# Kernel optimization log

Measured on AMD Instinct MI355X. Metric: run time of the kernel, lower is better.

Reference implementation:

```python
import jax, jax.numpy as jnp
import numpy as np

RATE = 2
KSIZE = 3
STRIDE = 1
SOFTMAX_SCALE = 10.0
EPS_NAN = 1e-4


def resize_bilinear_align(x, oh, ow):
    # torch F.interpolate(mode='bilinear', align_corners=True)
    B, C, H, W = x.shape
    ys = jnp.linspace(0.0, H - 1.0, oh)
    xs = jnp.linspace(0.0, W - 1.0, ow)
    y0 = jnp.floor(ys).astype(jnp.int32)
    y1 = jnp.minimum(y0 + 1, H - 1)
    wy = (ys - y0).astype(x.dtype)
    x0 = jnp.floor(xs).astype(jnp.int32)
    x1 = jnp.minimum(x0 + 1, W - 1)
    wx = (xs - x0).astype(x.dtype)
    t = x[:, :, y0, :] * (1 - wy)[None, None, :, None] + x[:, :, y1, :] * wy[None, None, :, None]
    return t[:, :, :, x0] * (1 - wx) + t[:, :, :, x1] * wx


def extract_patches(x, k, s, pad):
    # x: [C,H,W] -> [L, C, k, k] with SAME padding (pad on each side), L = oh*ow
    C, H, W = x.shape
    xp = jnp.pad(x, ((0, 0), (pad, pad), (pad, pad)))
    oh = (H + 2 * pad - k) // s + 1
    ow = (W + 2 * pad - k) // s + 1
    cols = jnp.stack(
        [xp[:, i:i + s * (oh - 1) + 1:s, j:j + s * (ow - 1) + 1:s]
         for i in range(k) for j in range(k)], axis=0)  # [k*k, C, oh, ow]
    return cols.reshape(k, k, C, oh, ow).transpose(3, 4, 2, 0, 1).reshape(oh * ow, C, k, k)


def conv2d(x, w, padding):
    # x: [N,C,H,W], w: [O,I,kh,kw]
    return jax.lax.conv_general_dilated(
        x, w, (1, 1), [(padding, padding)] * 2,
        dimension_numbers=('NCHW', 'OIHW', 'NCHW'))


def conv_transpose2d(x, w, stride, padding):
    # torch conv_transpose2d: x [N,I,h,w], w [I,O,kh,kw]
    k = w.shape[2]
    wt = jnp.flip(w, (2, 3)).transpose(1, 0, 2, 3)  # [O,I,kh,kw]
    return jax.lax.conv_general_dilated(
        x, wt, (1, 1), [(k - 1 - padding, k - 1 - padding)] * 2,
        lhs_dilation=(stride, stride),
        dimension_numbers=('NCHW', 'OIHW', 'NCHW'))


def setup_inputs() -> dict:
    key = jax.random.key(0)
    k1, k2 = jax.random.split(key)
    B, C, H, W = 4, 64, 128, 128
    background = jax.random.normal(k1, (B, C, H, W), dtype=jnp.float32)
    foreground = jax.random.normal(k2, (B, C, H, W), dtype=jnp.float32)
    return {"background": background, "foreground": foreground}


def reference(background, foreground):
    B, C, H, W = background.shape
    h, w = H // RATE, W // RATE
    fg = resize_bilinear_align(foreground, h, w)  # [B,C,h,w]
    bks = 2 * RATE  # background patch kernel = 4

    def per_sample(fg_i, bg_i):
        # foreground patches [L,C,3,3], L = h*w
        fgp = extract_patches(fg_i, KSIZE, STRIDE, 1)
        norm = jnp.sqrt(jnp.sum(fgp * fgp, axis=(1, 2, 3), keepdims=True))
        fgp_n = fgp / jnp.maximum(norm, EPS_NAN)
        # correlation score [1,L,h,w]
        score = conv2d(fg_i[None], fgp_n, padding=1)
        attn = jax.nn.softmax(score * SOFTMAX_SCALE, axis=1)
        attn = jnp.clip(attn, 1e-8, None)
        # background patches [L,C,4,4] (kernel 4, stride 2, same-pad 1)
        bgp = extract_patches(bg_i, bks, STRIDE * RATE, 1)
        out = conv_transpose2d(attn, bgp, stride=RATE, padding=1) / 4.0
        return out[0]  # [C,H,W]

    return jax.vmap(per_sample)(fg, background)
```

## Files before the change

kernel.cpp:

```cpp
#include <hip/hip_runtime.h>
#include <hip/hip_bf16.h>
#include <math.h>

#define B_  4
#define C_  64
#define H_  128
#define W_  128
#define HS  64
#define WS  64
#define L_  4096
#define K1  576
#define E2  1024
#define KSPLIT 1
#define ZLOG (-17.5f)

typedef _Float16 f16;
typedef f16 f16x8 __attribute__((ext_vector_type(8)));
typedef float f32x4 __attribute__((ext_vector_type(4)));

__device__ __forceinline__ void gload16(const void* g, void* l) {
    __builtin_amdgcn_global_load_lds(
        (const __attribute__((address_space(1))) unsigned int*)g,
        (__attribute__((address_space(3))) unsigned int*)l, 16, 0, 0);
}

__device__ __forceinline__ int swz(int r, int c) {
    return r * 128 + ((((c >> 3) ^ (r & 7)) << 3) | (c & 7));
}

__global__ __launch_bounds__(256) void resize_kernel(const float* __restrict__ fg,
                                                     float* __restrict__ fgs) {
    int idx = blockIdx.x * 256 + threadIdx.x;
    if (idx >= B_ * C_ * HS * WS) return;
    int j = idx & 63, i = (idx >> 6) & 63, bc = idx >> 12;
    const float sc = 127.0f / 63.0f;
    float yf = i * sc, xf = j * sc;
    int y0 = (int)floorf(yf); if (y0 > 127) y0 = 127;
    int x0 = (int)floorf(xf); if (x0 > 127) x0 = 127;
    int y1 = min(y0 + 1, 127), x1 = min(x0 + 1, 127);
    float wy = yf - (float)y0, wx = xf - (float)x0;
    const float* p = fg + (size_t)bc * (H_ * W_);
    float a = p[y0 * W_ + x0], b = p[y0 * W_ + x1];
    float c = p[y1 * W_ + x0], d = p[y1 * W_ + x1];
    float t0 = a * (1.f - wy) + c * wy;
    float t1 = b * (1.f - wy) + d * wy;
    fgs[idx] = t0 * (1.f - wx) + t1 * wx;
}

__global__ __launch_bounds__(256) void patch_kernel(const float* __restrict__ fgs,
                                                    f16* __restrict__ P_all) {
    int idx = blockIdx.x * 256 + threadIdx.x;
    int b = blockIdx.y;
    int k = idx % K1, l = idx / K1;
    int c = k / 9, r = k % 9;
    int dy = r / 3, dx = r % 3;
    int ly = l >> 6, lx = l & 63;
    int y = ly - 1 + dy, x = lx - 1 + dx;
    float v = 0.f;
    if ((unsigned)y < 64u && (unsigned)x < 64u)
        v = fgs[((size_t)b * C_ + c) * (HS * WS) + y * WS + x];
    P_all[(size_t)b * L_ * K1 + idx] = (f16)v;
}

__global__ __launch_bounds__(64) void norm_kernel(const f16* __restrict__ P_all,
                                                  float* __restrict__ nrm_all) {
    int l = blockIdx.x, b = blockIdx.y, t = threadIdx.x;
    const f16* row = P_all + ((size_t)b * L_ + l) * K1;
    float s = 0.f;
    for (int k = t; k < K1; k += 64) { float v = (float)row[k]; s = fmaf(v, v, s); }
    #pragma unroll
    for (int off = 32; off; off >>= 1) s += __shfl_down(s, off);
    if (t == 0) nrm_all[b * L_ + l] = fmaxf(sqrtf(s), 1e-4f);
}

__global__ __launch_bounds__(256) void v_kernel(const float* __restrict__ bg_g,
                                                f16* __restrict__ VT_g) {
    int ls = blockIdx.y;
    const float* bg_b = bg_g + (size_t)ls * (C_ * H_ * W_);
    f16* VT = VT_g + (size_t)ls * ((size_t)E2 * L_);
    int idx = blockIdx.x * 256 + threadIdx.x;
    int l = idx & 4095, e = idx >> 12;
    int c = e >> 4, r = e & 15;
    int ky = r >> 2, kx = r & 3;
    int ly = l >> 6, lx = l & 63;
    int by = 2 * ly - 1 + ky, bx = 2 * lx - 1 + kx;
    float v = 0.f;
    if ((unsigned)by < 128u && (unsigned)bx < 128u)
        v = bg_b[(size_t)c * (H_ * W_) + by * W_ + bx];
    VT[idx] = (f16)v;
}

__device__ __forceinline__ int nextk(int kn, int kLen, unsigned long long mask) {
    while (kn < kLen) {
        int t = kn >> 7;
        if (mask & (1ull << t)) return kn;
        unsigned long long m = mask >> t;
        if (!m) return kLen;
        kn = (t + __builtin_ctzll(m)) << 7;
    }
    return kn;
}

template <int EPI>
__global__ __launch_bounds__(512, 4)
void mfma_gemm(const f16* __restrict__ A, size_t sA,
               const f16* __restrict__ Bt, size_t sB,
               int lda, int ldb, int kLen, void* __restrict__ outp, size_t sOut,
               int ldc, const float* __restrict__ nrm, float* __restrict__ rowsum,
               int* __restrict__ flags) {
    __shared__ __align__(16) f16 As[2][2][128 * 32];
    __shared__ __align__(16) f16 Bs[2][2][128 * 32];
    __shared__ float sred[16];

    const int lin = blockIdx.x;
    const int S = gridDim.x >> 3;
    int bx, by, ls;
    if (EPI == 1) {
        int s = (lin & 7) * S + (lin >> 3);
        int R = s / 136, q = s - R * 136;
        ls = R >> 2;
        int rr = R & 3;
        if (rr < 2) {
            int a = 0;
            while (q >= 16 - a) { q -= 16 - a; ++a; }
            by = a + (rr << 4); bx = a + q + (rr << 4);
        } else {
            if (q >= 128) return;
            by = q & 15; bx = 16 + ((rr & 1) << 3) + (q >> 4);
        }
    } else {
        int G = (lin & 7) * S + (lin >> 3);
        ls = G >> 8;
        by = (G >> 5) & 7; bx = G & 31;
    }

    A  += (size_t)ls * sA;
    Bt += (size_t)ls * sB;
    f16* outbase = (f16*)outp + (size_t)ls * sOut;
    if (EPI == 1) { nrm += (size_t)ls * L_; rowsum += (size_t)ls * L_; }
    flags += ls * 1024;

    const int tid = threadIdx.x;
    const int w = tid >> 6, lane = tid & 63;
    const int row0 = by * 128, col0 = bx * 128;

    unsigned long long kmask = ~0ull;
    if (EPI == 0) {
        int f = (lane < 32) ? flags[bx * 32 + lane] : 0;
        kmask = __ballot(f != 0);
    }

    const int srow = tid >> 2;
    const int scol = (((tid & 3) ^ ((tid >> 3) & 3)) * 8);
    const f16* gA = A + (size_t)(row0 + srow) * lda + scol;
    const f16* gB = Bt + (size_t)(col0 + srow) * ldb + scol;
    const int ld = tid * 8;

    const int wm = w >> 2, wn = w & 3;
    const int mfm = lane & 15, quad = lane >> 4;
    const int rq = (quad ^ ((mfm >> 1) & 3)) * 8;
    f32x4 acc[4][2] = {};

    int kc = (EPI == 0) ? nextk(0, kLen, kmask) : 0;
    if (kc < kLen) {
        int cur = 0;
        gload16(gA + kc,      &As[0][0][ld]);
        gload16(gA + kc + 32, &As[0][1][ld]);
        gload16(gB + kc,      &Bs[0][0][ld]);
        gload16(gB + kc + 32, &Bs[0][1][ld]);
        for (;;) {
            int kn = (EPI == 0) ? nextk(kc + 64, kLen, kmask) : kc + 64;
            __builtin_amdgcn_s_barrier();
            if (kn < kLen) {
                const int nxt = cur ^ 1;
                gload16(gA + kn,      &As[nxt][0][ld]);
                gload16(gA + kn + 32, &As[nxt][1][ld]);
                gload16(gB + kn,      &Bs[nxt][0][ld]);
                gload16(gB + kn + 32, &Bs[nxt][1][ld]);
                asm volatile("s_waitcnt vmcnt(4)" ::: "memory");
            } else {
                asm volatile("s_waitcnt vmcnt(0)" ::: "memory");
            }
            __builtin_amdgcn_s_barrier();
            __builtin_amdgcn_sched_barrier(0);
            #pragma unroll
            for (int h = 0; h < 2; ++h) {
                f16x8 af[4], bf[2];
                #pragma unroll
                for (int mi = 0; mi < 4; ++mi)
                    af[mi] = *(const f16x8*)&As[cur][h][(wm * 64 + mi * 16 + mfm) * 32 + rq];
                #pragma unroll
                for (int ni = 0; ni < 2; ++ni)
                    bf[ni] = *(const f16x8*)&Bs[cur][h][(wn * 32 + ni * 16 + mfm) * 32 + rq];
                __builtin_amdgcn_s_setprio(1);
                #pragma unroll
                for (int mi = 0; mi < 4; ++mi)
                    #pragma unroll
                    for (int ni = 0; ni < 2; ++ni)
                        acc[mi][ni] = __builtin_amdgcn_mfma_f32_16x16x32_f16(
                            af[mi], bf[ni], acc[mi][ni], 0, 0, 0);
                __builtin_amdgcn_s_setprio(0);
            }
            cur ^= 1;
            kc = kn;
            if (kc >= kLen) break;
        }
    }

    const int orow = row0 + wm * 64;
    const int ocol = col0 + wn * 32;
    f16* st = &As[0][0][0];

    if (EPI == 1) {
        f16* Eo = outbase;
        const bool offd = (by != bx);
        float rowm[16], csr[16], cs[2], cm2[2];
        #pragma unroll
        for (int j = 0; j < 16; ++j) {
            float n = nrm[orow + (j >> 2) * 16 + quad * 4 + (j & 3)];
            rowm[j] = 10.0f * n; csr[j] = 10.0f / n;
        }
        #pragma unroll
        for (int ni = 0; ni < 2; ++ni) {
            float n = nrm[ocol + ni * 16 + mfm];
            cs[ni] = 10.0f / n; cm2[ni] = 10.0f * n;
        }
        float mx1 = -1e30f, mx2 = -1e30f;
        #pragma unroll
        for (int ni = 0; ni < 2; ++ni)
            #pragma unroll
            for (int mi = 0; mi < 4; ++mi)
                #pragma unroll
                for (int r = 0; r < 4; ++r) {
                    float a = acc[mi][ni][r];
                    mx1 = fmaxf(mx1, a * cs[ni] - rowm[mi * 4 + r]);
                    mx2 = fmaxf(mx2, a * csr[mi * 4 + r] - cm2[ni]);
                }
        #pragma unroll
        for (int off = 32; off; off >>= 1) {
            mx1 = fmaxf(mx1, __shfl_xor(mx1, off));
            mx2 = fmaxf(mx2, __shfl_xor(mx2, off));
        }
        if (lane == 0) { sred[w] = mx1; sred[8 + w] = mx2; }
        __syncthreads();
        float b1 = sred[0], b2 = sred[8];
        #pragma unroll
        for (int k = 1; k < 8; ++k) {
            b1 = fmaxf(b1, sred[k]); b2 = fmaxf(b2, sred[8 + k]);
        }
        int nz1 = b1 > ZLOG;
        int nz2 = offd && (b2 > ZLOG);
        if (nz1) {
            float rs[16] = {};
            #pragma unroll
            for (int ni = 0; ni < 2; ++ni)
                #pragma unroll
                for (int mi = 0; mi < 4; ++mi)
                    #pragma unroll
                    for (int r = 0; r < 4; ++r) {
                        float e = __expf(acc[mi][ni][r] * cs[ni] - rowm[mi * 4 + r]);
                        rs[mi * 4 + r] += e;
                        st[swz(wm * 64 + mi * 16 + quad * 4 + r,
                               wn * 32 + ni * 16 + mfm)] = (f16)e;
                    }
            __syncthreads();
            #pragma unroll
            for (int it = 0; it < 4; ++it) {
                int chunk = it * 512 + tid;
                int row = chunk >> 4, c16 = chunk & 15;
                f16x8 v = *(const f16x8*)&st[row * 128 + ((c16 ^ (row & 7)) << 3)];
                *(f16x8*)&Eo[(size_t)(row0 + row) * ldc + col0 + c16 * 8] = v;
            }
            #pragma unroll
            for (int j = 0; j < 16; ++j) {
                float v = rs[j];
                v += __shfl_xor(v, 1); v += __shfl_xor(v, 2);
                v += __shfl_xor(v, 4); v += __shfl_xor(v, 8);
                if (mfm == 0)
                    atomicAdd(&rowsum[orow + (j >> 2) * 16 + quad * 4 + (j & 3)], v);
            }
        }
        if (nz2) {
            __syncthreads();
            float rs2[2] = {};
            #pragma unroll
            for (int ni = 0; ni < 2; ++ni)
                #pragma unroll
                for (int mi = 0; mi < 4; ++mi)
                    #pragma unroll
                    for (int r = 0; r < 4; ++r) {
                        float e = __expf(acc[mi][ni][r] * csr[mi * 4 + r] - cm2[ni]);
                        rs2[ni] += e;
                        st[swz(wn * 32 + ni * 16 + mfm,
                               wm * 64 + mi * 16 + quad * 4 + r)] = (f16)e;
                    }
            __syncthreads();
            #pragma unroll
            for (int it = 0; it < 4; ++it) {
                int chunk = it * 512 + tid;
                int row = chunk >> 4, c16 = chunk & 15;
                f16x8 v = *(const f16x8*)&st[row * 128 + ((c16 ^ (row & 7)) << 3)];
                *(f16x8*)&Eo[(size_t)(col0 + row) * ldc + row0 + c16 * 8] = v;
            }
            #pragma unroll
            for (int ni = 0; ni < 2; ++ni) {
                float v = rs2[ni];
                v += __shfl_xor(v, 16); v += __shfl_xor(v, 32);
                if (quad == 0)
                    atomicAdd(&rowsum[ocol + ni * 16 + mfm], v);
            }
        }
        if (tid == 0) {
            flags[by * 32 + bx] = nz1;
            if (offd) flags[bx * 32 + by] = nz2;
        }
    } else {
        __syncthreads();
        #pragma unroll
        for (int ni = 0; ni < 2; ++ni)
            #pragma unroll
            for (int mi = 0; mi < 4; ++mi)
                #pragma unroll
                for (int r = 0; r < 4; ++r)
                    st[swz(wm * 64 + mi * 16 + quad * 4 + r,
                           wn * 32 + ni * 16 + mfm)] = (f16)acc[mi][ni][r];
        __syncthreads();
        f16* base = outbase + (size_t)row0 * ldc + col0;
        #pragma unroll
        for (int it = 0; it < 4; ++it) {
            int chunk = it * 512 + tid;
            int row = chunk >> 4, c16 = chunk & 15;
            f16x8 v = *(const f16x8*)&st[row * 128 + ((c16 ^ (row & 7)) << 3)];
            *(f16x8*)&base[(size_t)row * ldc + c16 * 8] = v;
        }
    }
}

__global__ __launch_bounds__(256) void gather_kernel(const f16* __restrict__ OPT_g,
                                                     const float* __restrict__ rowsum_g,
                                                     float* __restrict__ out_g) {
    int ls = blockIdx.y;
    const f16* OPT = OPT_g + (size_t)ls * ((size_t)KSPLIT * E2 * L_);
    const float* rowsum = rowsum_g + (size_t)ls * L_;
    float* out_b = out_g + (size_t)ls * (C_ * H_ * W_);
    int idx = blockIdx.x * 256 + threadIdx.x;
    if (idx >= C_ * H_ * W_) return;
    int X = idx & 127, Y = (idx >> 7) & 127, c = idx >> 14;
    int kyp = (Y + 1) & 1;
    int kxp = (X + 1) & 1;
    float sum = 0.f;
    #pragma unroll
    for (int ky = kyp; ky < 4; ky += 2) {
        int py = (Y + 1 - ky) >> 1;
        if ((unsigned)py >= 64u) continue;
        #pragma unroll
        for (int kx = kxp; kx < 4; kx += 2) {
            int px = (X + 1 - kx) >> 1;
            if ((unsigned)px >= 64u) continue;
            int p = py * 64 + px;
            int e = c * 16 + ky * 4 + kx;
            float v = 0.f;
            #pragma unroll
            for (int s = 0; s < KSPLIT; ++s)
                v += (float)OPT[((size_t)s * E2 + e) * L_ + p];
            sum += v * __builtin_amdgcn_rcpf(rowsum[p]);
        }
    }
    out_b[idx] = 0.25f * sum;
}

extern "C" void kernel_launch(void* const* d_in, const int* in_sizes, int n_in,
                              void* d_out, int out_size, void* d_ws, size_t ws_size,
                              hipStream_t stream) {
    const float* bg = (const float*)d_in[0];
    const float* fg = (const float*)d_in[1];
    float* out = (float*)d_out;
    char* w8 = (char*)d_ws;

    float* fgs        = (float*)(w8);
    f16*   P_all      = (f16*)  (w8 + 4194304);
    float* nrm        = (float*)(w8 + 23068672);
    float* rowsum_all = (float*)(w8 + 23134208);
    int*   flags      = (int*)  (w8 + 23199744);
    const size_t base = 23216128;

    const size_t perVT  = (size_t)E2 * L_ * 2;
    const size_t perEb  = (size_t)L_ * L_ * 2;
    const size_t perOPT = (size_t)KSPLIT * E2 * L_ * 2;
    const size_t per = perVT + perEb + perOPT;
    int nb = 1;
    if (ws_size >= base + 4 * per) nb = 4;
    else if (ws_size >= base + 2 * per) nb = 2;

    f16* VT  = (f16*)(w8 + base);
    f16* Eb  = (f16*)(w8 + base + (size_t)nb * perVT);
    f16* OPT = (f16*)(w8 + base + (size_t)nb * (perVT + perEb));

    resize_kernel<<<(B_ * C_ * HS * WS) / 256, 256, 0, stream>>>(fg, fgs);
    patch_kernel<<<dim3((L_ * K1) / 256, B_), 256, 0, stream>>>(fgs, P_all);
    norm_kernel<<<dim3(L_, B_), 64, 0, stream>>>(P_all, nrm);
    hipMemsetAsync(rowsum_all, 0, (size_t)B_ * L_ * sizeof(float), stream);

    for (int g = 0; g < B_; g += nb) {
        const f16* P_g     = P_all + (size_t)g * L_ * K1;
        const float* nrm_g = nrm + (size_t)g * L_;
        float* rowsum_g    = rowsum_all + (size_t)g * L_;
        int* flags_g       = flags + g * 1024;

        v_kernel<<<dim3((L_ * E2) / 256, nb), 256, 0, stream>>>(
            bg + (size_t)g * C_ * H_ * W_, VT);

        mfma_gemm<1><<<544 * nb, 512, 0, stream>>>(
            P_g, (size_t)L_ * K1, P_g, (size_t)L_ * K1,
            K1, K1, K1, Eb, (size_t)L_ * L_, L_,
            nrm_g, rowsum_g, flags_g);

        mfma_gemm<0><<<256 * nb, 512, 0, stream>>>(
            VT, (size_t)E2 * L_, Eb, (size_t)L_ * L_,
            L_, L_, L_, OPT, (size_t)KSPLIT * E2 * L_, L_,
            nullptr, nullptr, flags_g);

        gather_kernel<<<dim3((C_ * H_ * W_) / 256, nb), 256, 0, stream>>>(
            OPT, rowsum_g, out + (size_t)g * C_ * H_ * W_);
    }
}
```

Before: 233.7 us.

## Triple-buffer LDS tiles in MFMA GEMM main loop

Converts the GEMM K-loop from double to triple buffering so global-to-LDS loads are issued two stages ahead, with waitcnt thresholds adjusted to match. This aims to hide more global memory latency behind MFMA work. The extra LDS (96KB of tiles per block) forces launch bounds down to 2 blocks per CU, reducing occupancy. The barrier layout also changes, with one barrier moved after compute.

```diff
diff --git a/kernel.cpp b/kernel.cpp
--- a/kernel.cpp
+++ b/kernel.cpp
@@ -102,14 +102,14 @@
 }
 
 template <int EPI>
-__global__ __launch_bounds__(512, 4)
+__global__ __launch_bounds__(512, 2)
 void mfma_gemm(const f16* __restrict__ A, size_t sA,
                const f16* __restrict__ Bt, size_t sB,
                int lda, int ldb, int kLen, void* __restrict__ outp, size_t sOut,
                int ldc, const float* __restrict__ nrm, float* __restrict__ rowsum,
                int* __restrict__ flags) {
-    __shared__ __align__(16) f16 As[2][2][128 * 32];
-    __shared__ __align__(16) f16 Bs[2][2][128 * 32];
+    __shared__ __align__(16) f16 As[3][2][128 * 32];
+    __shared__ __align__(16) f16 Bs[3][2][128 * 32];
     __shared__ float sred[16];
 
     const int lin = blockIdx.x;
@@ -161,22 +161,28 @@
     const int rq = (quad ^ ((mfm >> 1) & 3)) * 8;
     f32x4 acc[4][2] = {};
 
-    int kc = (EPI == 0) ? nextk(0, kLen, kmask) : 0;
-    if (kc < kLen) {
+#define STAGE(b, k)                                   \
+    do {                                              \
+        gload16(gA + (k),      &As[b][0][ld]);        \
+        gload16(gA + (k) + 32, &As[b][1][ld]);        \
+        gload16(gB + (k),      &Bs[b][0][ld]);        \
+        gload16(gB + (k) + 32, &Bs[b][1][ld]);        \
+    } while (0)
+
+    int k0 = (EPI == 0) ? nextk(0, kLen, kmask) : 0;
+    if (k0 < kLen) {
+        int k1 = (EPI == 0) ? nextk(k0 + 64, kLen, kmask) : k0 + 64;
+        int k2 = (k1 < kLen) ? ((EPI == 0) ? nextk(k1 + 64, kLen, kmask) : k1 + 64)
+                             : kLen;
+        STAGE(0, k0);
+        if (k1 < kLen) STAGE(1, k1);
         int cur = 0;
-        gload16(gA + kc,      &As[0][0][ld]);
-        gload16(gA + kc + 32, &As[0][1][ld]);
-        gload16(gB + kc,      &Bs[0][0][ld]);
-        gload16(gB + kc + 32, &Bs[0][1][ld]);
         for (;;) {
-            int kn = (EPI == 0) ? nextk(kc + 64, kLen, kmask) : kc + 64;
-            __builtin_amdgcn_s_barrier();
-            if (kn < kLen) {
-                const int nxt = cur ^ 1;
-                gload16(gA + kn,      &As[nxt][0][ld]);
-                gload16(gA + kn + 32, &As[nxt][1][ld]);
-                gload16(gB + kn,      &Bs[nxt][0][ld]);
-                gload16(gB + kn + 32, &Bs[nxt][1][ld]);
+            int sb = cur + 2; if (sb >= 3) sb -= 3;
+            if (k2 < kLen) {
+                STAGE(sb, k2);
+                asm volatile("s_waitcnt vmcnt(8)" ::: "memory");
+            } else if (k1 < kLen) {
                 asm volatile("s_waitcnt vmcnt(4)" ::: "memory");
             } else {
                 asm volatile("s_waitcnt vmcnt(0)" ::: "memory");
@@ -201,11 +207,15 @@
                             af[mi], bf[ni], acc[mi][ni], 0, 0, 0);
                 __builtin_amdgcn_s_setprio(0);
             }
-            cur ^= 1;
-            kc = kn;
-            if (kc >= kLen) break;
-        }
-    }
+            __builtin_amdgcn_s_barrier();
+            if (k1 >= kLen) break;
+            k0 = k1; k1 = k2;
+            k2 = (k2 < kLen) ? ((EPI == 0) ? nextk(k2 + 64, kLen, kmask) : k2 + 64)
+                             : kLen;
+            cur += 1; if (cur >= 3) cur -= 3;
+        }
+    }
+#undef STAGE
 
     const int orow = row0 + wm * 64;
     const int ocol = col0 + wn * 32;
```

Result: slower. 266.1 us (+13.9%).

## Batch score GEMM across all samples and run per-sample AV GEMMs sequentially

Applied to the files above, without the earlier changes.

The score GEMM with softmax epilogue now runs once for all four samples (2176 blocks) into a workspace holding every sample's score matrix. The value-side work (V build, AV GEMM, gather) then loops per sample, reusing one VT/OPT buffer and launching 256 GEMM blocks each. Flags offsets move inside the EPI==1 branch, and the s_setprio around the MFMA block is removed. The fixed workspace layout assumes enough space for four score matrices, and the per-sample AV GEMMs give small grids that may underfill the GPU.

```diff
diff --git a/kernel.cpp b/kernel.cpp
--- a/kernel.cpp
+++ b/kernel.cpp
@@ -11,7 +11,6 @@
 #define L_  4096
 #define K1  576
 #define E2  1024
-#define KSPLIT 1
 #define ZLOG (-17.5f)
 
 typedef _Float16 f16;
@@ -73,11 +72,8 @@
     if (t == 0) nrm_all[b * L_ + l] = fmaxf(sqrtf(s), 1e-4f);
 }
 
-__global__ __launch_bounds__(256) void v_kernel(const float* __restrict__ bg_g,
-                                                f16* __restrict__ VT_g) {
-    int ls = blockIdx.y;
-    const float* bg_b = bg_g + (size_t)ls * (C_ * H_ * W_);
-    f16* VT = VT_g + (size_t)ls * ((size_t)E2 * L_);
+__global__ __launch_bounds__(256) void v_kernel(const float* __restrict__ bg_b,
+                                                f16* __restrict__ VT) {
     int idx = blockIdx.x * 256 + threadIdx.x;
     int l = idx & 4095, e = idx >> 12;
     int c = e >> 4, r = e & 15;
@@ -137,8 +133,10 @@
     A  += (size_t)ls * sA;
     Bt += (size_t)ls * sB;
     f16* outbase = (f16*)outp + (size_t)ls * sOut;
-    if (EPI == 1) { nrm += (size_t)ls * L_; rowsum += (size_t)ls * L_; }
-    flags += ls * 1024;
+    if (EPI == 1) {
+        nrm += (size_t)ls * L_; rowsum += (size_t)ls * L_;
+        flags += ls * 1024;
+    }
 
     const int tid = threadIdx.x;
     const int w = tid >> 6, lane = tid & 63;
@@ -192,14 +190,12 @@
                 #pragma unroll
                 for (int ni = 0; ni < 2; ++ni)
                     bf[ni] = *(const f16x8*)&Bs[cur][h][(wn * 32 + ni * 16 + mfm) * 32 + rq];
-                __builtin_amdgcn_s_setprio(1);
                 #pragma unroll
                 for (int mi = 0; mi < 4; ++mi)
                     #pragma unroll
                     for (int ni = 0; ni < 2; ++ni)
                         acc[mi][ni] = __builtin_amdgcn_mfma_f32_16x16x32_f16(
                             af[mi], bf[ni], acc[mi][ni], 0, 0, 0);
-                __builtin_amdgcn_s_setprio(0);
             }
             cur ^= 1;
             kc = kn;
@@ -336,13 +332,9 @@
     }
 }
 
-__global__ __launch_bounds__(256) void gather_kernel(const f16* __restrict__ OPT_g,
-                                                     const float* __restrict__ rowsum_g,
-                                                     float* __restrict__ out_g) {
-    int ls = blockIdx.y;
-    const f16* OPT = OPT_g + (size_t)ls * ((size_t)KSPLIT * E2 * L_);
-    const float* rowsum = rowsum_g + (size_t)ls * L_;
-    float* out_b = out_g + (size_t)ls * (C_ * H_ * W_);
+__global__ __launch_bounds__(256) void gather_kernel(const f16* __restrict__ OPT,
+                                                     const float* __restrict__ rowsum,
+                                                     float* __restrict__ out_b) {
     int idx = blockIdx.x * 256 + threadIdx.x;
     if (idx >= C_ * H_ * W_) return;
     int X = idx & 127, Y = (idx >> 7) & 127, c = idx >> 14;
@@ -359,10 +351,7 @@
             if ((unsigned)px >= 64u) continue;
             int p = py * 64 + px;
             int e = c * 16 + ky * 4 + kx;
-            float v = 0.f;
-            #pragma unroll
-            for (int s = 0; s < KSPLIT; ++s)
-                v += (float)OPT[((size_t)s * E2 + e) * L_ + p];
+            float v = (float)OPT[(size_t)e * L_ + p];
             sum += v * __builtin_amdgcn_rcpf(rowsum[p]);
         }
     }
@@ -384,43 +373,35 @@
     int*   flags      = (int*)  (w8 + 23199744);
     const size_t base = 23216128;
 
-    const size_t perVT  = (size_t)E2 * L_ * 2;
-    const size_t perEb  = (size_t)L_ * L_ * 2;
-    const size_t perOPT = (size_t)KSPLIT * E2 * L_ * 2;
-    const size_t per = perVT + perEb + perOPT;
-    int nb = 1;
-    if (ws_size >= base + 4 * per) nb = 4;
-    else if (ws_size >= base + 2 * per) nb = 2;
-
-    f16* VT  = (f16*)(w8 + base);
-    f16* Eb  = (f16*)(w8 + base + (size_t)nb * perVT);
-    f16* OPT = (f16*)(w8 + base + (size_t)nb * (perVT + perEb));
+    const size_t EB_ELEMS = (size_t)L_ * L_;
+    f16* Eb_all = (f16*)(w8 + base);
+    f16* VT     = (f16*)(w8 + base + 4 * EB_ELEMS * 2);
+    f16* OPT    = (f16*)(w8 + base + 4 * EB_ELEMS * 2 + (size_t)E2 * L_ * 2);
 
     resize_kernel<<<(B_ * C_ * HS * WS) / 256, 256, 0, stream>>>(fg, fgs);
     patch_kernel<<<dim3((L_ * K1) / 256, B_), 256, 0, stream>>>(fgs, P_all);
     norm_kernel<<<dim3(L_, B_), 64, 0, stream>>>(P_all, nrm);
     hipMemsetAsync(rowsum_all, 0, (size_t)B_ * L_ * sizeof(float), stream);
 
-    for (int g = 0; g < B_; g += nb) {
-        const f16* P_g     = P_all + (size_t)g * L_ * K1;
-        const float* nrm_g = nrm + (size_t)g * L_;
-        float* rowsum_g    = rowsum_all + (size_t)g * L_;
-        int* flags_g       = flags + g * 1024;
-
-        v_kernel<<<dim3((L_ * E2) / 256, nb), 256, 0, stream>>>(
-            bg + (size_t)g * C_ * H_ * W_, VT);
-
-        mfma_gemm<1><<<544 * nb, 512, 0, stream>>>(
-            P_g, (size_t)L_ * K1, P_g, (size_t)L_ * K1,
-            K1, K1, K1, Eb, (size_t)L_ * L_, L_,
-            nrm_g, rowsum_g, flags_g);
-
-        mfma_gemm<0><<<256 * nb, 512, 0, stream>>>(
-            VT, (size_t)E2 * L_, Eb, (size_t)L_ * L_,
-            L_, L_, L_, OPT, (size_t)KSPLIT * E2 * L_, L_,
-            nullptr, nullptr, flags_g);
-
-        gather_kernel<<<dim3((C_ * H_ * W_) / 256, nb), 256, 0, stream>>>(
-            OPT, rowsum_g, out + (size_t)g * C_ * H_ * W_);
-    }
-}
+    mfma_gemm<1><<<2176, 512, 0, stream>>>(
+        P_all, (size_t)L_ * K1, P_all, (size_t)L_ * K1,
+        K1, K1, K1, Eb_all, EB_ELEMS, L_,
+        nrm, rowsum_all, flags);
+
+    for (int b = 0; b < B_; ++b) {
+        const f16* Eb_b    = Eb_all + (size_t)b * EB_ELEMS;
+        const float* rs_b  = rowsum_all + (size_t)b * L_;
+        int* flags_b       = flags + b * 1024;
+
+        v_kernel<<<(L_ * E2) / 256, 256, 0, stream>>>(
+            bg + (size_t)b * C_ * H_ * W_, VT);
+
+        mfma_gemm<0><<<256, 512, 0, stream>>>(
+            VT, 0, Eb_b, 0,
+            L_, L_, L_, OPT, 0, L_,
+            nullptr, nullptr, flags_b);
+
+        gather_kernel<<<(C_ * H_ * W_) / 256, 256, 0, stream>>>(
+            OPT, rs_b, out + (size_t)b * C_ * H_ * W_);
+    }
+}
```

After: 266.1 us. 1.14x slower.
